# Kernel tuning notes

Measured on AMD Instinct MI355X. Metric: run time of the kernel, lower is better.

Reference implementation:

```python
import jax, jax.numpy as jnp
import numpy as np
import math

PATCH = 41
NUM_ANG = 8
NUM_SPATIAL = 4
BIN_KSIZE = 2 * int(PATCH / (NUM_SPATIAL + 1))   # 16
BIN_STRIDE = PATCH // NUM_SPATIAL                # 10
BIN_PAD = BIN_KSIZE // 4                         # 4
CLIPVAL = 0.2
EPS = 1e-10
N = 8192


def _sift_pooling_kernel(ksize: int) -> np.ndarray:
    k2 = float(ksize) / 2.0
    xc2 = k2 - np.abs(np.arange(ksize, dtype=np.float32) + 0.5 - k2)
    return (np.outer(xc2, xc2) / k2 ** 2).astype(np.float32)


def _sift_weighting_kernel(ksize: int) -> np.ndarray:
    # Gauss, vlfeat sigma: sigma_mul_2 = ksize**2
    k2 = float(ksize) / 2.0
    ys = np.arange(ksize, dtype=np.float32)[:, None]
    xs = np.arange(ksize, dtype=np.float32)[None, :]
    disq = (ys - k2 + 0.5) ** 2 + (xs - k2 + 0.5) ** 2
    return np.exp(-disq / float(ksize ** 2)).astype(np.float32)


def setup_inputs() -> dict:
    key = jax.random.key(0)
    x = jax.random.normal(key, (N, 1, PATCH, PATCH), dtype=jnp.float32)
    gk = jnp.asarray(_sift_weighting_kernel(PATCH))   # [41,41]
    pk = jnp.asarray(_sift_pooling_kernel(BIN_KSIZE))  # [16,16]
    return {"x": x, "gk": gk, "pk": pk}


def _l2_normalize(v):
    return v / jnp.maximum(jnp.linalg.norm(v, axis=1, keepdims=True), 1e-12)


def reference(x, gk, pk):
    # gradients via replicate-pad + central difference (matches [-1,0,1] convs)
    xp = jnp.pad(x, ((0, 0), (0, 0), (0, 0), (1, 1)), mode='edge')
    gx = xp[..., 2:] - xp[..., :-2]
    yp = jnp.pad(x, ((0, 0), (0, 0), (1, 1), (0, 0)), mode='edge')
    gy = yp[:, :, 2:, :] - yp[:, :, :-2, :]

    mag = jnp.sqrt(gx * gx + gy * gy + EPS) * gk  # gaussian-weighted magnitude
    ori = jnp.arctan2(gy, gx + EPS)

    # soft angular binning
    o_big = (ori + 2.0 * math.pi) / (2.0 * math.pi) * NUM_ANG
    bo0f = jnp.floor(o_big)
    wo1 = o_big - bo0f
    bo0 = bo0f.astype(jnp.int32) % NUM_ANG
    bo1 = (bo0 + 1) % NUM_ANG
    # [N,1,P,P,nb]
    contrib = (jax.nn.one_hot(bo0, NUM_ANG, dtype=mag.dtype) * ((1.0 - wo1) * mag)[..., None]
               + jax.nn.one_hot(bo1, NUM_ANG, dtype=mag.dtype) * (wo1 * mag)[..., None])
    contrib = jnp.transpose(contrib[:, 0], (0, 3, 1, 2))  # [N,nb,P,P]

    # depthwise weighted spatial pooling (same triangular kernel per angular bin)
    kern = jnp.broadcast_to(pk[None, None], (NUM_ANG, 1, BIN_KSIZE, BIN_KSIZE))
    pooled = jax.lax.conv_general_dilated(
        contrib, kern,
        window_strides=(BIN_STRIDE, BIN_STRIDE),
        padding=[(BIN_PAD, BIN_PAD), (BIN_PAD, BIN_PAD)],
        feature_group_count=NUM_ANG,
        dimension_numbers=('NCHW', 'OIHW', 'NCHW'))  # [N,nb,4,4]

    desc = pooled.reshape(pooled.shape[0], -1)  # [N,128]
    desc = _l2_normalize(desc)
    desc = jnp.clip(desc, 0.0, CLIPVAL)
    desc = _l2_normalize(desc)
    # rootsift: sqrt of L1-normalized descriptor
    desc = desc / jnp.maximum(jnp.sum(jnp.abs(desc), axis=1, keepdims=True), 1e-12)
    return jnp.sqrt(desc + 1e-10)
```

## Files before the change

### kernel.cpp

```cpp
#include <hip/hip_runtime.h>
#include <hip/hip_fp16.h>
#include <math.h>

#define PATCH 41
#define PP 1681
#define NB 8
#define STRIDE 10
#define PAD 4
#define NTH 256
#define CPIX (PP + 14)
#define XROW 44
#define XSZ (PATCH * XROW)

__device__ __forceinline__ constexpr float tri16(int k) {
    float d = (float)k + 0.5f - 8.0f;
    float a = d < 0.0f ? -d : d;
    return (8.0f - a) * 0.125f;
}

__device__ __forceinline__ void load4(const __half* s, int k,
                                      float& f0, float& f1, float& f2, float& f3) {
    __half2 lo = *(const __half2*)&s[k];
    __half2 hi = *(const __half2*)&s[k + 2];
    f0 = __low2float(lo);  f1 = __high2float(lo);
    f2 = __low2float(hi);  f3 = __high2float(hi);
}

__device__ __forceinline__ uint4 pixel_contrib(float gx, float gy, float gauss) {
    float X = gx + 1e-10f;
    float mag = __builtin_amdgcn_sqrtf(fmaf(gx, gx, fmaf(gy, gy, 1e-10f))) * gauss;

    float ax = fabsf(X), ay = fabsf(gy);
    float mx = fmaxf(ax, ay), mn = fminf(ax, ay);
    float r = mn * __builtin_amdgcn_rcpf(fmaxf(mx, 1e-30f));
    float r2 = r * r;
    float a4 = fmaf(r2, -0.0149238f, 0.0670406f);
    a4 = fmaf(r2, a4, -0.1482457f);
    a4 = fmaf(r2, a4, 0.2464287f);
    a4 = fmaf(r2, a4, -0.4235106f);
    a4 = fmaf(r2, a4, 1.2732106f);
    a4 *= r;

    bool sw = ay > ax;
    bool xn = X < 0.0f;
    bool yn = gy < 0.0f;
    int q = (xn ? 2 : 0) + ((sw != xn) ? 1 : 0);
    int b0 = yn ? 7 - q : q;
    bool f = (sw != xn) != yn;
    float ma = a4 * mag;
    float mb = mag - ma;
    float v0 = f ? ma : mb;
    float v1 = f ? mb : ma;

    unsigned combo = __builtin_bit_cast(unsigned, __builtin_amdgcn_cvt_pkrtz(v0, v1));
    int sh = (b0 & 3) << 4;
    unsigned long long A = (unsigned long long)combo << sh;
    unsigned long long B = ((b0 & 3) == 3) ? (unsigned long long)(combo >> 16) : 0ull;
    bool lohalf = b0 < 4;
    unsigned long long lo = lohalf ? A : B;
    unsigned long long hi = lohalf ? B : A;
    uint4 cw;
    cw.x = (unsigned)lo; cw.y = (unsigned)(lo >> 32);
    cw.z = (unsigned)hi; cw.w = (unsigned)(hi >> 32);
    return cw;
}

__global__ __launch_bounds__(NTH, 5) void sift_desc_kernel(
        const float* __restrict__ x,
        const float* __restrict__ gk,
        const float* __restrict__ pk,
        float* __restrict__ out)
{
    const int patch = blockIdx.x;
    const int t = threadIdx.x;

    __shared__ __align__(16) __half s_c[CPIX * NB];
    __shared__ __align__(16) __half s_xp[XSZ];
    __shared__ float s_rc[PATCH];
    __half* s_H = s_xp;
    float* s_desc = reinterpret_cast<float*>(s_c);

    if (t < PATCH) {
        float d = (float)(t - 20);
        s_rc[t] = __builtin_amdgcn_exp2f(d * d * -8.582362e-4f);
    }
    const float* xp = x + (size_t)patch * PP;
    for (int idx = t; idx < XSZ; idx += NTH) {
        int i = idx / XROW;
        int jj = idx - i * XROW - 1;
        int jc = min(max(jj, 0), PATCH - 1);
        s_xp[idx] = __float2half(xp[i * PATCH + jc]);
    }
    if (t < 14) {
        uint4 z; z.x = z.y = z.z = z.w = 0u;
        int idx = (t < 4) ? t : (PP + t);
        *(uint4*)&s_c[idx * NB] = z;
    }
    __syncthreads();

    if (t < 231) {
        const int strip = t / 21;
        const int pairc = t - strip * 21;
        const int j = 2 * pairc;
        const int i0 = 4 * strip;
        const float cf0 = s_rc[j];
        const float cf1 = s_rc[min(j + 1, PATCH - 1)];
        const bool has1 = (j < PATCH - 1);

        const int kMax = (PATCH - 1) * XROW + j;
        int kA = max(i0 - 1, 0) * XROW + j;
        int kB = i0 * XROW + j;
        float A0, A1, A2, A3, B0, B1, B2, B3;
        load4(s_xp, kA, A0, A1, A2, A3);
        load4(s_xp, kB, B0, B1, B2, B3);
        int kC = min(kB + XROW, kMax);
        int pbase = (i0 * PATCH + j + 4) * NB;

        #pragma unroll
        for (int r = 0; r < 4; ++r) {
            const int i = i0 + r;
            const bool ok = (i < PATCH);
            float C0, C1, C2, C3;
            load4(s_xp, kC, C0, C1, C2, C3);
            float rf = s_rc[min(i, PATCH - 1)];

            uint4 cw0 = pixel_contrib(B2 - B0, C1 - A1, rf * cf0);
            uint4 cw1 = pixel_contrib(B3 - B1, C2 - A2, rf * cf1);
            if (ok) {
                *(uint4*)&s_c[pbase] = cw0;
                if (has1) *(uint4*)&s_c[pbase + NB] = cw1;
            }

            A0 = B0; A1 = B1; A2 = B2; A3 = B3;
            B0 = C0; B1 = C1; B2 = C2; B3 = C3;
            kC = min(kC + XROW, kMax);
            pbase += PATCH * NB;
        }
    }
    __syncthreads();

    if (t < PATCH * 4) {
        const int row = t >> 2;
        const int ox = t & 3;
        const int sbase = row * PATCH + ox * STRIDE;
        const __half2 z2 = __float2half2_rn(0.0f);
        __half2 a0 = z2, a1 = z2, a2 = z2, a3 = z2;
        #pragma unroll
        for (int kx = 0; kx < 16; ++kx) {
            const float w = tri16(kx);
            __half2 wp = __float2half2_rn(w);
            if (kx < PAD)  wp = (ox > 0) ? wp : z2;
            if (kx == 15)  wp = (ox < 3) ? wp : z2;
            uint4 cwv = *(const uint4*)&s_c[(sbase + kx) * NB];
            a0 = __hfma2(wp, *(__half2*)&cwv.x, a0);
            a1 = __hfma2(wp, *(__half2*)&cwv.y, a1);
            a2 = __hfma2(wp, *(__half2*)&cwv.z, a2);
            a3 = __hfma2(wp, *(__half2*)&cwv.w, a3);
        }
        uint4 hv;
        hv.x = *(unsigned*)&a0;
        hv.y = *(unsigned*)&a1;
        hv.z = *(unsigned*)&a2;
        hv.w = *(unsigned*)&a3;
        *(uint4*)&s_H[(row * 4 + ox) * NB] = hv;
    }
    __syncthreads();

    float v = 0.0f;
    if (t < 128) {
        int b = t >> 4;
        int oy = (t >> 2) & 3;
        int ox = t & 3;
        #pragma unroll
        for (int ky = 0; ky < 16; ++ky) {
            const float w = tri16(ky);
            int iy = oy * STRIDE - PAD + ky;
            int iyc = min(max(iy, 0), PATCH - 1);
            float hv = __half2float(s_H[(iyc * 4 + ox) * NB + b]);
            v = fmaf((iy == iyc) ? w : 0.0f, hv, v);
        }
        s_desc[t] = v;
    }
    __syncthreads();

    if (t < 64) {
        float a = s_desc[t];
        float b = s_desc[t + 64];

        float ss = fmaf(a, a, b * b);
        #pragma unroll
        for (int o = 32; o > 0; o >>= 1) ss += __shfl_xor(ss, o);
        float inv = 1.0f / fmaxf(__builtin_amdgcn_sqrtf(ss), 1e-12f);
        a = fminf(fmaxf(a * inv, 0.0f), 0.2f);
        b = fminf(fmaxf(b * inv, 0.0f), 0.2f);

        float ss2 = fmaf(a, a, b * b);
        #pragma unroll
        for (int o = 32; o > 0; o >>= 1) ss2 += __shfl_xor(ss2, o);
        float inv2 = 1.0f / fmaxf(__builtin_amdgcn_sqrtf(ss2), 1e-12f);
        a *= inv2; b *= inv2;

        float l1 = a + b;
        #pragma unroll
        for (int o = 32; o > 0; o >>= 1) l1 += __shfl_xor(l1, o);
        float invl = 1.0f / fmaxf(l1, 1e-12f);

        float* op = out + (size_t)patch * 128;
        op[t]      = __builtin_amdgcn_sqrtf(fmaf(a, invl, 1e-10f));
        op[t + 64] = __builtin_amdgcn_sqrtf(fmaf(b, invl, 1e-10f));
    }
}

extern "C" void kernel_launch(void* const* d_in, const int* in_sizes, int n_in,
                              void* d_out, int out_size, void* d_ws, size_t ws_size,
                              hipStream_t stream) {
    const float* x  = (const float*)d_in[0];
    const float* gk = (const float*)d_in[1];
    const float* pk = (const float*)d_in[2];
    float* out = (float*)d_out;
    const int n = in_sizes[0] / PP;
    sift_desc_kernel<<<n, NTH, 0, stream>>>(x, gk, pk, out);
}
```

Measured before the change: 123.3 us.

## Fuse gradient/orientation binning into horizontal pooling pass, dropping contribution buffer

Removes the intermediate per-pixel contribution array in shared memory and its separate pass. Each horizontal-pooling thread now computes gradients and soft-binned contributions for its 16-pixel window directly from the padded half-precision patch, folding the pooling weight into the magnitude. Pixels in overlapping windows are recomputed, about 1.6x more atan work, but a barrier and a large LDS store/load round trip go away. Block size drops to 192 threads and occupancy rises, helped by the smaller LDS footprint.

```diff
diff --git a/kernel.cpp b/kernel.cpp
--- a/kernel.cpp
+++ b/kernel.cpp
@@ -7,23 +7,14 @@
 #define NB 8
 #define STRIDE 10
 #define PAD 4
-#define NTH 256
-#define CPIX (PP + 14)
-#define XROW 44
+#define NTH 192
+#define XROW 52
 #define XSZ (PATCH * XROW)
 
 __device__ __forceinline__ constexpr float tri16(int k) {
     float d = (float)k + 0.5f - 8.0f;
     float a = d < 0.0f ? -d : d;
     return (8.0f - a) * 0.125f;
-}
-
-__device__ __forceinline__ void load4(const __half* s, int k,
-                                      float& f0, float& f1, float& f2, float& f3) {
-    __half2 lo = *(const __half2*)&s[k];
-    __half2 hi = *(const __half2*)&s[k + 2];
-    f0 = __low2float(lo);  f1 = __high2float(lo);
-    f2 = __low2float(hi);  f3 = __high2float(hi);
 }
 
 __device__ __forceinline__ uint4 pixel_contrib(float gx, float gy, float gauss) {
@@ -65,7 +56,7 @@
     return cw;
 }
 
-__global__ __launch_bounds__(NTH, 5) void sift_desc_kernel(
+__global__ __launch_bounds__(NTH, 6) void sift_desc_kernel(
         const float* __restrict__ x,
         const float* __restrict__ gk,
         const float* __restrict__ pk,
@@ -74,89 +65,76 @@
     const int patch = blockIdx.x;
     const int t = threadIdx.x;
 
-    __shared__ __align__(16) __half s_c[CPIX * NB];
     __shared__ __align__(16) __half s_xp[XSZ];
-    __shared__ float s_rc[PATCH];
-    __half* s_H = s_xp;
-    float* s_desc = reinterpret_cast<float*>(s_c);
-
-    if (t < PATCH) {
-        float d = (float)(t - 20);
-        s_rc[t] = __builtin_amdgcn_exp2f(d * d * -8.582362e-4f);
-    }
+    __shared__ __align__(16) __half s_cw[XROW];
+    __shared__ __align__(16) __half s_H[PATCH * 4 * NB];
+    __shared__ float s_desc[128];
+
     const float* xp = x + (size_t)patch * PP;
     for (int idx = t; idx < XSZ; idx += NTH) {
         int i = idx / XROW;
-        int jj = idx - i * XROW - 1;
-        int jc = min(max(jj, 0), PATCH - 1);
+        int c = idx - i * XROW - 6;
+        int jc = min(max(c, 0), PATCH - 1);
         s_xp[idx] = __float2half(xp[i * PATCH + jc]);
     }
-    if (t < 14) {
-        uint4 z; z.x = z.y = z.z = z.w = 0u;
-        int idx = (t < 4) ? t : (PP + t);
-        *(uint4*)&s_c[idx * NB] = z;
-    }
-    __syncthreads();
-
-    if (t < 231) {
-        const int strip = t / 21;
-        const int pairc = t - strip * 21;
-        const int j = 2 * pairc;
-        const int i0 = 4 * strip;
-        const float cf0 = s_rc[j];
-        const float cf1 = s_rc[min(j + 1, PATCH - 1)];
-        const bool has1 = (j < PATCH - 1);
-
-        const int kMax = (PATCH - 1) * XROW + j;
-        int kA = max(i0 - 1, 0) * XROW + j;
-        int kB = i0 * XROW + j;
-        float A0, A1, A2, A3, B0, B1, B2, B3;
-        load4(s_xp, kA, A0, A1, A2, A3);
-        load4(s_xp, kB, B0, B1, B2, B3);
-        int kC = min(kB + XROW, kMax);
-        int pbase = (i0 * PATCH + j + 4) * NB;
-
-        #pragma unroll
-        for (int r = 0; r < 4; ++r) {
-            const int i = i0 + r;
-            const bool ok = (i < PATCH);
-            float C0, C1, C2, C3;
-            load4(s_xp, kC, C0, C1, C2, C3);
-            float rf = s_rc[min(i, PATCH - 1)];
-
-            uint4 cw0 = pixel_contrib(B2 - B0, C1 - A1, rf * cf0);
-            uint4 cw1 = pixel_contrib(B3 - B1, C2 - A2, rf * cf1);
-            if (ok) {
-                *(uint4*)&s_c[pbase] = cw0;
-                if (has1) *(uint4*)&s_c[pbase + NB] = cw1;
-            }
-
-            A0 = B0; A1 = B1; A2 = B2; A3 = B3;
-            B0 = C0; B1 = C1; B2 = C2; B3 = C3;
-            kC = min(kC + XROW, kMax);
-            pbase += PATCH * NB;
-        }
+    if (t < XROW) {
+        float dj = (float)(t - 26);
+        s_cw[t] = __float2half(__builtin_amdgcn_exp2f(dj * dj * -8.582362e-4f));
     }
     __syncthreads();
 
     if (t < PATCH * 4) {
         const int row = t >> 2;
         const int ox = t & 3;
-        const int sbase = row * PATCH + ox * STRIDE;
+        const int jw0 = ox * STRIDE - PAD;
+        const int base = jw0 + 6;
+        const int rowM = row * XROW;
+        const int rowU = (row > 0 ? row - 1 : 0) * XROW;
+        const int rowD = (row < PATCH - 1 ? row + 1 : PATCH - 1) * XROW;
+        const bool zlo = (ox == 0);
+        const bool zhi = (ox == 3);
+
+        float drow = (float)(row - 20);
+        const float rf = __builtin_amdgcn_exp2f(drow * drow * -8.582362e-4f);
+
+        __half2 pmh = *(const __half2*)&s_xp[rowM + base - 2];
+        __half2 cmh = *(const __half2*)&s_xp[rowM + base];
+        float pm0 = __low2float(pmh), pm1 = __high2float(pmh);
+        float cm0 = __low2float(cmh), cm1 = __high2float(cmh);
+
         const __half2 z2 = __float2half2_rn(0.0f);
         __half2 a0 = z2, a1 = z2, a2 = z2, a3 = z2;
-        #pragma unroll
-        for (int kx = 0; kx < 16; ++kx) {
-            const float w = tri16(kx);
-            __half2 wp = __float2half2_rn(w);
-            if (kx < PAD)  wp = (ox > 0) ? wp : z2;
-            if (kx == 15)  wp = (ox < 3) ? wp : z2;
-            uint4 cwv = *(const uint4*)&s_c[(sbase + kx) * NB];
-            a0 = __hfma2(wp, *(__half2*)&cwv.x, a0);
-            a1 = __hfma2(wp, *(__half2*)&cwv.y, a1);
-            a2 = __hfma2(wp, *(__half2*)&cwv.z, a2);
-            a3 = __hfma2(wp, *(__half2*)&cwv.w, a3);
+
+        #pragma unroll
+        for (int it = 0; it < 8; ++it) {
+            const int kx0 = 2 * it;
+            __half2 nmh = *(const __half2*)&s_xp[rowM + base + kx0 + 2];
+            __half2 uh  = *(const __half2*)&s_xp[rowU + base + kx0];
+            __half2 dh  = *(const __half2*)&s_xp[rowD + base + kx0];
+            __half2 cwh = *(const __half2*)&s_cw[base + kx0];
+
+            __half2 gyh = __hsub2(dh, uh);
+            float gy0 = __low2float(gyh), gy1 = __high2float(gyh);
+            float nm0 = __low2float(nmh), nm1 = __high2float(nmh);
+            float cf0 = __low2float(cwh), cf1 = __high2float(cwh);
+
+            float w0 = tri16(kx0);
+            float w1 = tri16(kx0 + 1);
+            if (kx0 < 4)      { w0 = zlo ? 0.0f : w0; w1 = zlo ? 0.0f : w1; }
+            if (kx0 + 1 == 15){ w1 = zhi ? 0.0f : w1; }
+
+            uint4 c0 = pixel_contrib(cm1 - pm1, gy0, rf * (w0 * cf0));
+            uint4 c1 = pixel_contrib(nm0 - cm0, gy1, rf * (w1 * cf1));
+
+            a0 = __hadd2(a0, __hadd2(*(__half2*)&c0.x, *(__half2*)&c1.x));
+            a1 = __hadd2(a1, __hadd2(*(__half2*)&c0.y, *(__half2*)&c1.y));
+            a2 = __hadd2(a2, __hadd2(*(__half2*)&c0.z, *(__half2*)&c1.z));
+            a3 = __hadd2(a3, __hadd2(*(__half2*)&c0.w, *(__half2*)&c1.w));
+
+            pm0 = cm0; pm1 = cm1;
+            cm0 = nm0; cm1 = nm1;
         }
+
         uint4 hv;
         hv.x = *(unsigned*)&a0;
         hv.y = *(unsigned*)&a1;
@@ -166,11 +144,11 @@
     }
     __syncthreads();
 
-    float v = 0.0f;
     if (t < 128) {
         int b = t >> 4;
         int oy = (t >> 2) & 3;
         int ox = t & 3;
+        float v = 0.0f;
         #pragma unroll
         for (int ky = 0; ky < 16; ++ky) {
             const float w = tri16(ky);
```

After: 125.3 us. About the same (+1.6%).
